# Kernel tuning notes

Measured on AMD Instinct MI355X. Metric: run time of the kernel, lower is better.

The kernel has to match this reference:

```python
import jax, jax.numpy as jnp
import numpy as np

N, E, B = 20000, 320000, 128
IN_DIM, HID, HEADS = 64, 64, 4
D = HID * HEADS          # 256 = conv output width (concat heads)
CAT = HID + 2 * D        # 576 = dueling head input
ENC_H, DUEL_H = 512, 128
NEG_SLOPE = 0.2


def setup_inputs() -> dict:
    key = jax.random.key(0)
    ks = jax.random.split(key, 30)
    g = lambda i, shape: jax.random.normal(ks[i], shape, dtype=jnp.float32) * 0.05
    return {
        "x": jax.random.normal(ks[0], (N, IN_DIM), dtype=jnp.float32),
        "edge_index": jax.random.randint(ks[1], (2, E), 0, N, dtype=jnp.int32),
        "indices": jax.random.randint(ks[2], (B,), 0, N, dtype=jnp.int32),
        # encoder MLP: input_dim -> 512 -> hidden_dim
        "enc_w1": g(3, (IN_DIM, ENC_H)), "enc_b1": g(4, (ENC_H,)),
        "enc_w2": g(5, (ENC_H, HID)),   "enc_b2": g(6, (HID,)),
        # GATv2 conv1: HID -> HID per head, HEADS heads
        "wl1": g(7, (HID, D)),  "bl1": g(8, (D,)),
        "wr1": g(9, (HID, D)),  "br1": g(10, (D,)),
        "att1": g(11, (HEADS, HID)), "bias1": g(12, (D,)),
        # GATv2 conv2: D -> HID per head, HEADS heads
        "wl2": g(13, (D, D)),   "bl2": g(14, (D,)),
        "wr2": g(15, (D, D)),   "br2": g(16, (D,)),
        "att2": g(17, (HEADS, HID)), "bias2": g(18, (D,)),
        # dueling heads: CAT -> 128 -> {2, 1}
        "q_w1": g(19, (CAT, DUEL_H)), "q_b1": g(20, (DUEL_H,)),
        "q_w2": g(21, (DUEL_H, 2)),   "q_b2": g(22, (2,)),
        "v_w1": g(23, (CAT, DUEL_H)), "v_b1": g(24, (DUEL_H,)),
        "v_w2": g(25, (DUEL_H, 1)),   "v_b2": g(26, (1,)),
    }


def _gatv2(h, src, dst, wl, bl, wr, br, att, bias):
    # PyG GATv2Conv: e_ij = att . leaky_relu(Wl h_j + Wr h_i); softmax over
    # incoming edges of each target i; out_i = sum_j alpha_ij * (Wl h_j).
    xl = (h @ wl + bl).reshape(-1, HEADS, HID)  # source transform
    xr = (h @ wr + br).reshape(-1, HEADS, HID)  # target transform
    e = jax.nn.leaky_relu(xl[src] + xr[dst], NEG_SLOPE)      # [E', H, D]
    score = jnp.einsum('ehd,hd->eh', e, att)                 # [E', H]
    m = jax.ops.segment_max(score, dst, num_segments=N)      # stable softmax
    ex = jnp.exp(score - m[dst])
    denom = jax.ops.segment_sum(ex, dst, num_segments=N)
    alpha = ex / (denom[dst] + 1e-16)                        # [E', H]
    out = jax.ops.segment_sum(alpha[:, :, None] * xl[src], dst, num_segments=N)
    return out.reshape(-1, D) + bias


def _forward(x, edge_index, indices,
             enc_w1, enc_b1, enc_w2, enc_b2,
             wl1, bl1, wr1, br1, att1, bias1,
             wl2, bl2, wr2, br2, att2, bias2,
             q_w1, q_b1, q_w2, q_b2, v_w1, v_b1, v_w2, v_b2):
    loops = jnp.arange(N, dtype=edge_index.dtype)  # add_self_loops=True
    src = jnp.concatenate([edge_index[0], loops])
    dst = jnp.concatenate([edge_index[1], loops])

    h = jax.nn.relu(x @ enc_w1 + enc_b1)
    h = jax.nn.relu(h @ enc_w2 + enc_b2)          # encoder + F.relu
    x1 = h[indices]
    h = jax.nn.relu(_gatv2(h, src, dst, wl1, bl1, wr1, br1, att1, bias1))
    x2 = h[indices]
    h = jax.nn.relu(_gatv2(h, src, dst, wl2, bl2, wr2, br2, att2, bias2))
    x3 = h[indices]

    feat = jnp.concatenate([x1, x2, x3], axis=1)  # [B, CAT]
    q = jax.nn.relu(feat @ q_w1 + q_b1) @ q_w2 + q_b2  # [B, 2]
    v = jax.nn.relu(feat @ v_w1 + v_b1) @ v_w2 + v_b2  # [B, 1]
    return q - q.mean(axis=1, keepdims=True) + v


def reference(x, edge_index, indices,
              enc_w1, enc_b1, enc_w2, enc_b2,
              wl1, bl1, wr1, br1, att1, bias1,
              wl2, bl2, wr2, br2, att2, bias2,
              q_w1, q_b1, q_w2, q_b2, v_w1, v_b1, v_w2, v_b2):
    return _forward(x, edge_index, indices,
                    enc_w1, enc_b1, enc_w2, enc_b2,
                    wl1, bl1, wr1, br1, att1, bias1,
                    wl2, bl2, wr2, br2, att2, bias2,
                    q_w1, q_b1, q_w2, q_b2, v_w1, v_b1, v_w2, v_b2)
```

## Files before the change

kernel.cpp:

```cpp
#include <hip/hip_runtime.h>

#define IN_DIM 64
#define HID 64
#define HEADS 4
#define DD 256
#define ENC_H 512
#define DUEL_H 128
#define NEG_SLOPE 0.2f
#define WCAP 8192
#define ECAP 64

typedef _Float16 f16;
typedef __attribute__((ext_vector_type(2))) _Float16 f16x2;
typedef __attribute__((ext_vector_type(4))) _Float16 f16x4;
typedef __attribute__((ext_vector_type(8))) _Float16 f16x8;
typedef __attribute__((ext_vector_type(4))) float f32x4;

__device__ __forceinline__ f16x2 u2h(unsigned u) {
    union { unsigned u; f16x2 h; } c; c.u = u; return c.h;
}
__device__ __forceinline__ unsigned h2u(f16x2 h) {
    union { unsigned u; f16x2 h; } c; c.h = h; return c.u;
}


__global__ void prep_all(
    const float4* __restrict__ x, f16x4* __restrict__ x16, int nx4,
    const float* __restrict__ w1, const float* __restrict__ w2,
    const float* __restrict__ wl1, const float* __restrict__ wr1,
    const float* __restrict__ wl2, const float* __restrict__ wr2,
    f16* __restrict__ w1t, f16* __restrict__ w2t,
    f16* __restrict__ wcat1, f16* __restrict__ wcat2,
    f16* __restrict__ wr2nt,
    int* __restrict__ zeros, int nz) {
    int i = blockIdx.x * blockDim.x + threadIdx.x;
    if (i < nx4) {
        float4 v = x[i];
        f16x4 o = {(f16)v.x, (f16)v.y, (f16)v.z, (f16)v.w};
        x16[i] = o;
        return;
    }
    i -= nx4;
    if (i < 229376) {
        if (i < 32768) {
            int k = i >> 9, n = i & 511;
            w1t[n * 64 + k] = (f16)w1[i];
        } else if (i < 65536) {
            int j = i - 32768; int k = j >> 6, n = j & 63;
            w2t[n * 512 + k] = (f16)w2[j];
        } else if (i < 81920) {
            int j = i - 65536; int k = j >> 8, n = j & 255;
            wcat1[n * 64 + k] = (f16)wl1[j];
        } else if (i < 98304) {
            int j = i - 81920; int k = j >> 8, n = j & 255;
            wcat1[(256 + n) * 64 + k] = (f16)wr1[j];
        } else if (i < 163840) {
            int j = i - 98304; int k = j >> 8, n = j & 255;
            wcat2[n * 256 + k] = (f16)wl2[j];
        } else {
            int j = i - 163840;
            wr2nt[j] = (f16)wr2[j];
        }
        return;
    }
    i -= 229376;
    if (i < nz) zeros[i] = 0;
}


template <int K, int BN>
struct GemmCfg {
    static constexpr int SB = K + 8;
    static constexpr int CE = BN / 2 + 8;
    static constexpr int SLABSZ = BN * SB;
    static constexpr int EPISZ = 4 * 32 * CE;
    static constexpr int SMEMSZ = SLABSZ > EPISZ ? SLABSZ : EPISZ;
};

template <int K, int BN>
__device__ __forceinline__ void gemm_body(
    int bx, int by, f16* __restrict__ smem,
    const f16* __restrict__ A, const f16* __restrict__ Bt,
    const float* __restrict__ biasA, const float* __restrict__ biasB, int NS,
    int M, int relu,
    f16* __restrict__ C1, f16* __restrict__ C2) {
    constexpr int KS = K / 32;
    constexpr int PF = (KS < 8) ? KS : 8;
    constexpr int COLW = BN / 2;
    constexpr int NT = COLW / 16;
    constexpr int SB = GemmCfg<K, BN>::SB;
    constexpr int CE = GemmCfg<K, BN>::CE;

    f16* Bs = smem;
    int tid = threadIdx.x;
    int wave = tid >> 6, lane = tid & 63;
    int quad = lane >> 4, l16 = lane & 15;
    int wr = wave >> 1, wc = wave & 1;
    int row0 = by * 64;
    int col0 = bx * BN;

    constexpr int NCH = BN * K / 8;
#pragma unroll
    for (int i = 0; i < NCH / 256; ++i) {
        int c = tid + i * 256;
        int r = c / (K / 8), ko = (c % (K / 8)) * 8;
        uint4 v = *(const uint4*)&Bt[(size_t)(col0 + r) * K + ko];
        *(uint4*)&Bs[r * SB + ko] = v;
    }
    __syncthreads();

    const f16* Aptr[2];
#pragma unroll
    for (int mt = 0; mt < 2; ++mt) {
        int arow = row0 + wr * 32 + mt * 16 + l16;
        if (arow >= M) arow = M - 1;
        Aptr[mt] = &A[(size_t)arow * K + quad * 8];
    }

    f32x4 acc[2][NT];
#pragma unroll
    for (int mt = 0; mt < 2; ++mt)
#pragma unroll
        for (int j = 0; j < NT; ++j) acc[mt][j] = (f32x4){0.f, 0.f, 0.f, 0.f};

    f16x8 afb[2][PF];
#pragma unroll
    for (int mt = 0; mt < 2; ++mt)
#pragma unroll
        for (int i = 0; i < PF; ++i)
            afb[mt][i] = *(const f16x8*)&Aptr[mt][i * 32];

#pragma unroll
    for (int s = 0; s < KS; ++s) {
        f16x8 af0 = afb[0][s % PF], af1 = afb[1][s % PF];
        if (s + PF < KS) {
            afb[0][s % PF] = *(const f16x8*)&Aptr[0][(s + PF) * 32];
            afb[1][s % PF] = *(const f16x8*)&Aptr[1][(s + PF) * 32];
        }
        const f16* bbase = &Bs[(size_t)(wc * COLW) * SB + s * 32 + quad * 8];
#pragma unroll
        for (int nt = 0; nt < NT; ++nt) {
            f16x8 bf = *(const f16x8*)&bbase[(nt * 16 + l16) * SB];
            acc[0][nt] = __builtin_amdgcn_mfma_f32_16x16x32_f16(af0, bf, acc[0][nt], 0, 0, 0);
            acc[1][nt] = __builtin_amdgcn_mfma_f32_16x16x32_f16(af1, bf, acc[1][nt], 0, 0, 0);
        }
    }

    __syncthreads();
    f16* ep = &smem[wave * 32 * CE];
#pragma unroll
    for (int mt = 0; mt < 2; ++mt)
#pragma unroll
        for (int nt = 0; nt < NT; ++nt) {
            int gcol = col0 + wc * COLW + nt * 16 + l16;
            float bb = (gcol < NS) ? biasA[gcol] : biasB[gcol - NS];
#pragma unroll
            for (int r = 0; r < 4; ++r) {
                float v = acc[mt][nt][r] + bb;
                if (relu) v = fmaxf(v, 0.f);
                ep[(mt * 16 + quad * 4 + r) * CE + nt * 16 + l16] = (f16)v;
            }
        }
    constexpr int CPR = COLW / 8;
    constexpr int NPASS = (32 * CPR) / 64;
#pragma unroll
    for (int i = 0; i < NPASS; ++i) {
        int u = lane + i * 64;
        int row = u / CPR, seg = u % CPR;
        uint4 v = *(const uint4*)&ep[row * CE + seg * 8];
        int grow = row0 + wr * 32 + row;
        int gcol = col0 + wc * COLW + seg * 8;
        if (grow < M) {
            if (gcol < NS) *(uint4*)&C1[(size_t)grow * NS + gcol] = v;
            else           *(uint4*)&C2[(size_t)grow * NS + (gcol - NS)] = v;
        }
    }
}


__global__ __launch_bounds__(256) void conv2t_gather_kernel(
    const f16* __restrict__ A, const f16* __restrict__ Bt,
    const float* __restrict__ bias,
    const int* __restrict__ wlist, const int* __restrict__ wcnt,
    f16* __restrict__ C) {
    constexpr int K = 256, BN = 128;
    constexpr int KS = K / 32, PF = 8;
    constexpr int COLW = BN / 2, NT = COLW / 16;
    constexpr int SB = GemmCfg<K, BN>::SB;
    constexpr int CE = GemmCfg<K, BN>::CE;
    __shared__ __align__(16) f16 smem[GemmCfg<K, BN>::SMEMSZ];

    int M_c = wcnt[0];
    int row0 = blockIdx.y * 64;
    if (row0 >= M_c) return;

    f16* Bs = smem;
    int tid = threadIdx.x;
    int wave = tid >> 6, lane = tid & 63;
    int quad = lane >> 4, l16 = lane & 15;
    int wr = wave >> 1, wc = wave & 1;
    int col0 = blockIdx.x * BN;

    constexpr int NCH = BN * K / 8;
#pragma unroll
    for (int i = 0; i < NCH / 256; ++i) {
        int c = tid + i * 256;
        int r = c / (K / 8), ko = (c % (K / 8)) * 8;
        uint4 v = *(const uint4*)&Bt[(size_t)(col0 + r) * K + ko];
        *(uint4*)&Bs[r * SB + ko] = v;
    }
    __syncthreads();

    const f16* Aptr[2];
#pragma unroll
    for (int mt = 0; mt < 2; ++mt) {
        int crow = row0 + wr * 32 + mt * 16 + l16;
        if (crow >= M_c) crow = M_c - 1;
        int arow = wlist[crow];
        Aptr[mt] = &A[(size_t)arow * K + quad * 8];
    }

    f32x4 acc[2][NT];
#pragma unroll
    for (int mt = 0; mt < 2; ++mt)
#pragma unroll
        for (int j = 0; j < NT; ++j) acc[mt][j] = (f32x4){0.f, 0.f, 0.f, 0.f};

    f16x8 afb[2][PF];
#pragma unroll
    for (int mt = 0; mt < 2; ++mt)
#pragma unroll
        for (int i = 0; i < PF; ++i)
            afb[mt][i] = *(const f16x8*)&Aptr[mt][i * 32];

#pragma unroll
    for (int s = 0; s < KS; ++s) {
        f16x8 af0 = afb[0][s % PF], af1 = afb[1][s % PF];
        const f16* bbase = &Bs[(size_t)(wc * COLW) * SB + s * 32 + quad * 8];
#pragma unroll
        for (int nt = 0; nt < NT; ++nt) {
            f16x8 bf = *(const f16x8*)&bbase[(nt * 16 + l16) * SB];
            acc[0][nt] = __builtin_amdgcn_mfma_f32_16x16x32_f16(af0, bf, acc[0][nt], 0, 0, 0);
            acc[1][nt] = __builtin_amdgcn_mfma_f32_16x16x32_f16(af1, bf, acc[1][nt], 0, 0, 0);
        }
    }

    __syncthreads();
    f16* ep = &smem[wave * 32 * CE];
#pragma unroll
    for (int mt = 0; mt < 2; ++mt)
#pragma unroll
        for (int nt = 0; nt < NT; ++nt) {
            int gcol = col0 + wc * COLW + nt * 16 + l16;
            float bb = bias[gcol];
#pragma unroll
            for (int r = 0; r < 4; ++r)
                ep[(mt * 16 + quad * 4 + r) * CE + nt * 16 + l16] =
                    (f16)(acc[mt][nt][r] + bb);
        }
    constexpr int CPR = COLW / 8;
    constexpr int NPASS = (32 * CPR) / 64;
#pragma unroll
    for (int i = 0; i < NPASS; ++i) {
        int u = lane + i * 64;
        int row = u / CPR, seg = u % CPR;
        uint4 v = *(const uint4*)&ep[row * CE + seg * 8];
        int grow = row0 + wr * 32 + row;
        int gcol = col0 + wc * COLW + seg * 8;
        if (grow < M_c) *(uint4*)&C[(size_t)grow * DD + gcol] = v;
    }
}


__device__ __forceinline__ void wappend(int src, int* __restrict__ inW,
                                        int* __restrict__ wcnt,
                                        int* __restrict__ wlist,
                                        int* __restrict__ mapv,
                                        int* __restrict__ w_edges,
                                        int* __restrict__ ecnt) {
    if (atomicExch(&inW[src], 1) == 0) {
        int c = atomicAdd(wcnt, 1);
        if (c < WCAP) {
            wlist[c] = src;
            mapv[src] = c;
            w_edges[c * ECAP] = src;
            ecnt[c] = 1;
        }
    }
}

__global__ __launch_bounds__(256) void enc1_s0_kernel(
    const f16* __restrict__ A, const f16* __restrict__ Bt,
    const float* __restrict__ bias, int M, f16* __restrict__ C, int gemmBlocks,
    const int* __restrict__ indices, int B,
    int* __restrict__ s0f, int* __restrict__ inW, int* __restrict__ wcnt,
    int* __restrict__ wlist, int* __restrict__ mapv,
    int* __restrict__ w_edges, int* __restrict__ ecnt) {
    __shared__ __align__(16) f16 smem[GemmCfg<64, 128>::SMEMSZ];
    int bid = blockIdx.x;
    if (bid >= gemmBlocks) {
        int t = threadIdx.x;
        if (t < B) {
            int src = indices[t];
            s0f[src] = 1;
            wappend(src, inW, wcnt, wlist, mapv, w_edges, ecnt);
        }
        return;
    }
    gemm_body<64, 128>(bid & 3, bid >> 2, smem, A, Bt, bias, bias, 512, M, 1, C, C);
}

__global__ __launch_bounds__(256) void enc2_wscan_kernel(
    const f16* __restrict__ A, const f16* __restrict__ Bt,
    const float* __restrict__ bias, int M, f16* __restrict__ C, int gemmBlocks,
    const int* __restrict__ ei, int E,
    const int* __restrict__ s0f, int* __restrict__ inW, int* __restrict__ wcnt,
    int* __restrict__ wlist, int* __restrict__ mapv,
    int* __restrict__ w_edges, int* __restrict__ ecnt) {
    __shared__ __align__(16) f16 smem[GemmCfg<512, 64>::SMEMSZ];
    int bid = blockIdx.x;
    if (bid < gemmBlocks) {
        gemm_body<512, 64>(0, bid, smem, A, Bt, bias, bias, 64, M, 1, C, C);
    } else {
        int e = (bid - gemmBlocks) * 256 + threadIdx.x;
        if (e < E) {
            int dst = ei[E + e];
            if (s0f[dst])
                wappend(ei[e], inW, wcnt, wlist, mapv, w_edges, ecnt);
        }
    }
}

__global__ __launch_bounds__(256) void conv1t_ebuild_kernel(
    const f16* __restrict__ A, const f16* __restrict__ Bt,
    const float* __restrict__ biasA, const float* __restrict__ biasB, int M,
    f16* __restrict__ C1, f16* __restrict__ C2, int gemmBlocks,
    const int* __restrict__ ei, int E,
    const int* __restrict__ inW, const int* __restrict__ mapv,
    int* __restrict__ w_edges, int* __restrict__ ecnt) {
    __shared__ __align__(16) f16 smem[GemmCfg<64, 128>::SMEMSZ];
    int bid = blockIdx.x;
    if (bid < gemmBlocks) {
        gemm_body<64, 128>(bid & 3, bid >> 2, smem, A, Bt, biasA, biasB, DD, M, 0, C1, C2);
    } else {
        int e = (bid - gemmBlocks) * 256 + threadIdx.x;
        if (e < E) {
            int dst = ei[E + e];
            if (inW[dst]) {
                int c = mapv[dst];
                int pos = atomicAdd(&ecnt[c], 1);
                if (pos < ECAP) w_edges[c * ECAP + pos] = ei[e];
            }
        }
    }
}


__global__ __launch_bounds__(256) void gat_fused_kernel(
    const uint4* __restrict__ xl, const uint4* __restrict__ xr,
    const float4* __restrict__ att,
    const int* __restrict__ wlist, const int* __restrict__ wcnt,
    const int* __restrict__ w_edges, const int* __restrict__ ecnt,
    const float4* __restrict__ bias, uint4* __restrict__ h16) {
    int w = (blockIdx.x * blockDim.x + threadIdx.x) >> 6;
    int lane = threadIdx.x & 63;
    int half = lane >> 5, l32 = lane & 31;
    if (w >= wcnt[0]) return;
    int node = wlist[w];
    int L = ecnt[w];
    if (L > ECAP) L = ECAP;
    const int* elist = &w_edges[w * ECAP];
    uint4 xrw = xr[(size_t)node * 32 + l32];
    f16x2 xr0 = u2h(xrw.x), xr1 = u2h(xrw.y), xr2 = u2h(xrw.z), xr3 = u2h(xrw.w);
    float4 awA = att[l32 * 2], awB = att[l32 * 2 + 1];
    f16x2 a6[4] = {{(f16)(0.6f * awA.x), (f16)(0.6f * awA.y)},
                   {(f16)(0.6f * awA.z), (f16)(0.6f * awA.w)},
                   {(f16)(0.6f * awB.x), (f16)(0.6f * awB.y)},
                   {(f16)(0.6f * awB.z), (f16)(0.6f * awB.w)}};
    f16x2 a4[4] = {{(f16)(0.4f * awA.x), (f16)(0.4f * awA.y)},
                   {(f16)(0.4f * awA.z), (f16)(0.4f * awA.w)},
                   {(f16)(0.4f * awB.x), (f16)(0.4f * awB.y)},
                   {(f16)(0.4f * awB.z), (f16)(0.4f * awB.w)}};
    float denom = 0.f;
    float acc0 = 0.f, acc1 = 0.f, acc2 = 0.f, acc3 = 0.f;
    float acc4 = 0.f, acc5 = 0.f, acc6 = 0.f, acc7 = 0.f;

    auto edge_dot = [&](uint4 raw) -> float {
        f16x2 t0 = u2h(raw.x) + xr0, t1 = u2h(raw.y) + xr1;
        f16x2 t2 = u2h(raw.z) + xr2, t3 = u2h(raw.w) + xr3;
        float d = __builtin_amdgcn_fdot2(t0, a6[0], 0.f, false);
        d = __builtin_amdgcn_fdot2(u2h(h2u(t0) & 0x7FFF7FFFu), a4[0], d, false);
        d = __builtin_amdgcn_fdot2(t1, a6[1], d, false);
        d = __builtin_amdgcn_fdot2(u2h(h2u(t1) & 0x7FFF7FFFu), a4[1], d, false);
        d = __builtin_amdgcn_fdot2(t2, a6[2], d, false);
        d = __builtin_amdgcn_fdot2(u2h(h2u(t2) & 0x7FFF7FFFu), a4[2], d, false);
        d = __builtin_amdgcn_fdot2(t3, a6[3], d, false);
        d = __builtin_amdgcn_fdot2(u2h(h2u(t3) & 0x7FFF7FFFu), a4[3], d, false);
        return d;
    };
    auto accum = [&](uint4 raw, float ee) {
        f16x2 v0 = u2h(raw.x), v1 = u2h(raw.y), v2 = u2h(raw.z), v3 = u2h(raw.w);
        acc0 = fmaf(ee, (float)v0.x, acc0); acc1 = fmaf(ee, (float)v0.y, acc1);
        acc2 = fmaf(ee, (float)v1.x, acc2); acc3 = fmaf(ee, (float)v1.y, acc3);
        acc4 = fmaf(ee, (float)v2.x, acc4); acc5 = fmaf(ee, (float)v2.y, acc5);
        acc6 = fmaf(ee, (float)v3.x, acc6); acc7 = fmaf(ee, (float)v3.y, acc7);
    };

    int p = half;
    for (; p + 6 < L; p += 8) {
        uint4 raw[4];
#pragma unroll
        for (int j = 0; j < 4; ++j)
            raw[j] = xl[(size_t)elist[p + j * 2] * 32 + l32];
        float sc[4];
#pragma unroll
        for (int j = 0; j < 4; ++j) sc[j] = edge_dot(raw[j]);
#pragma unroll
        for (int j = 0; j < 4; ++j) sc[j] += __shfl_xor(sc[j], 1);
#pragma unroll
        for (int j = 0; j < 4; ++j) sc[j] += __shfl_xor(sc[j], 2);
#pragma unroll
        for (int j = 0; j < 4; ++j) sc[j] += __shfl_xor(sc[j], 4);
#pragma unroll
        for (int j = 0; j < 4; ++j) {
            float ee = __expf(sc[j]);
            denom += ee;
            accum(raw[j], ee);
        }
    }
    for (; p < L; p += 2) {
        uint4 raw = xl[(size_t)elist[p] * 32 + l32];
        float d = edge_dot(raw);
        d += __shfl_xor(d, 1);
        d += __shfl_xor(d, 2);
        d += __shfl_xor(d, 4);
        float ee = __expf(d);
        denom += ee;
        accum(raw, ee);
    }
    denom += __shfl_xor(denom, 32);
    acc0 += __shfl_xor(acc0, 32); acc1 += __shfl_xor(acc1, 32);
    acc2 += __shfl_xor(acc2, 32); acc3 += __shfl_xor(acc3, 32);
    acc4 += __shfl_xor(acc4, 32); acc5 += __shfl_xor(acc5, 32);
    acc6 += __shfl_xor(acc6, 32); acc7 += __shfl_xor(acc7, 32);

    if (half == 0) {
        float inv = 1.f / (denom + 1e-16f);
        float4 bbA = bias[l32 * 2], bbB = bias[l32 * 2 + 1];
        float o0 = fmaxf(fmaf(acc0, inv, bbA.x), 0.f);
        float o1 = fmaxf(fmaf(acc1, inv, bbA.y), 0.f);
        float o2 = fmaxf(fmaf(acc2, inv, bbA.z), 0.f);
        float o3 = fmaxf(fmaf(acc3, inv, bbA.w), 0.f);
        float o4 = fmaxf(fmaf(acc4, inv, bbB.x), 0.f);
        float o5 = fmaxf(fmaf(acc5, inv, bbB.y), 0.f);
        float o6 = fmaxf(fmaf(acc6, inv, bbB.z), 0.f);
        float o7 = fmaxf(fmaf(acc7, inv, bbB.w), 0.f);
        f16x2 h0 = {(f16)o0, (f16)o1}, h1 = {(f16)o2, (f16)o3};
        f16x2 h2 = {(f16)o4, (f16)o5}, h3 = {(f16)o6, (f16)o7};
        uint4 outw = make_uint4(h2u(h0), h2u(h1), h2u(h2), h2u(h3));
        h16[(size_t)node * 32 + l32] = outw;
    }
}


__global__ __launch_bounds__(1024) void gat2_head_kernel(
    const uint4* __restrict__ xl, const f16* __restrict__ hC1,
    const f16* __restrict__ wr2nt, const float* __restrict__ br2,
    const float4* __restrict__ att,
    const int* __restrict__ indices, const int* __restrict__ mapv,
    const int* __restrict__ w_edges, const int* __restrict__ ecnt,
    const float* __restrict__ bias2, const f16* __restrict__ hE16,
    const float* __restrict__ qw1, const float* __restrict__ qb1,
    const float* __restrict__ qw2, const float* __restrict__ qb2,
    const float* __restrict__ vw1, const float* __restrict__ vb1,
    const float* __restrict__ vw2, const float* __restrict__ vb2,
    float* __restrict__ out) {
    __shared__ float feat[576];
    __shared__ float xrs[256];
    __shared__ float partial[4][256];
    __shared__ float pden[16][32];
    __shared__ float pacc[16][32][8];
    __shared__ float red[384];
    int b = blockIdx.x;
    int t = threadIdx.x;
    int wave = t >> 6, lane = t & 63;
    int half = lane >> 5, l32 = lane & 31;
    int node = indices[b];

    if (t < 320) {
        feat[t] = (t < 64) ? (float)hE16[(size_t)node * 64 + t]
                           : (float)hC1[(size_t)node * 256 + t - 64];
    }
    __syncthreads();

    {
        int o = t & 255, kq = t >> 8;
        const f16* w = &wr2nt[(size_t)(kq * 64) * 256 + o];
        const float* f = &feat[64 + kq * 64];
        float a0 = 0.f, a1 = 0.f;
#pragma unroll
        for (int k = 0; k < 64; k += 2) {
            a0 = fmaf(f[k],     (float)w[(size_t)k * 256],       a0);
            a1 = fmaf(f[k + 1], (float)w[(size_t)(k + 1) * 256], a1);
        }
        partial[kq][o] = a0 + a1;
    }
    __syncthreads();
    if (t < 256)
        xrs[t] = partial[0][t] + partial[1][t] + partial[2][t] + partial[3][t] + br2[t];
    __syncthreads();

    f16x2 xr0 = {(f16)xrs[l32 * 8 + 0], (f16)xrs[l32 * 8 + 1]};
    f16x2 xr1 = {(f16)xrs[l32 * 8 + 2], (f16)xrs[l32 * 8 + 3]};
    f16x2 xr2 = {(f16)xrs[l32 * 8 + 4], (f16)xrs[l32 * 8 + 5]};
    f16x2 xr3 = {(f16)xrs[l32 * 8 + 6], (f16)xrs[l32 * 8 + 7]};

    int cidx0 = mapv[node];
    int L = ecnt[cidx0];
    if (L > ECAP) L = ECAP;
    const int* elist = &w_edges[cidx0 * ECAP];
    float4 awA = att[l32 * 2], awB = att[l32 * 2 + 1];
    f16x2 a6[4] = {{(f16)(0.6f * awA.x), (f16)(0.6f * awA.y)},
                   {(f16)(0.6f * awA.z), (f16)(0.6f * awA.w)},
                   {(f16)(0.6f * awB.x), (f16)(0.6f * awB.y)},
                   {(f16)(0.6f * awB.z), (f16)(0.6f * awB.w)}};
    f16x2 a4[4] = {{(f16)(0.4f * awA.x), (f16)(0.4f * awA.y)},
                   {(f16)(0.4f * awA.z), (f16)(0.4f * awA.w)},
                   {(f16)(0.4f * awB.x), (f16)(0.4f * awB.y)},
                   {(f16)(0.4f * awB.z), (f16)(0.4f * awB.w)}};
    float denom = 0.f;
    float acc0 = 0.f, acc1 = 0.f, acc2 = 0.f, acc3 = 0.f;
    float acc4 = 0.f, acc5 = 0.f, acc6 = 0.f, acc7 = 0.f;

    auto edge_dot = [&](uint4 raw) -> float {
        f16x2 t0 = u2h(raw.x) + xr0, t1 = u2h(raw.y) + xr1;
        f16x2 t2 = u2h(raw.z) + xr2, t3 = u2h(raw.w) + xr3;
        float d = __builtin_amdgcn_fdot2(t0, a6[0], 0.f, false);
        d = __builtin_amdgcn_fdot2(u2h(h2u(t0) & 0x7FFF7FFFu), a4[0], d, false);
        d = __builtin_amdgcn_fdot2(t1, a6[1], d, false);
        d = __builtin_amdgcn_fdot2(u2h(h2u(t1) & 0x7FFF7FFFu), a4[1], d, false);
        d = __builtin_amdgcn_fdot2(t2, a6[2], d, false);
        d = __builtin_amdgcn_fdot2(u2h(h2u(t2) & 0x7FFF7FFFu), a4[2], d, false);
        d = __builtin_amdgcn_fdot2(t3, a6[3], d, false);
        d = __builtin_amdgcn_fdot2(u2h(h2u(t3) & 0x7FFF7FFFu), a4[3], d, false);
        return d;
    };
    auto accum = [&](uint4 raw, float ee) {
        f16x2 v0 = u2h(raw.x), v1 = u2h(raw.y), v2 = u2h(raw.z), v3 = u2h(raw.w);
        acc0 = fmaf(ee, (float)v0.x, acc0); acc1 = fmaf(ee, (float)v0.y, acc1);
        acc2 = fmaf(ee, (float)v1.x, acc2); acc3 = fmaf(ee, (float)v1.y, acc3);
        acc4 = fmaf(ee, (float)v2.x, acc4); acc5 = fmaf(ee, (float)v2.y, acc5);
        acc6 = fmaf(ee, (float)v3.x, acc6); acc7 = fmaf(ee, (float)v3.y, acc7);
    };

    for (int p = (wave << 1) + half; p < L; p += 32) {
        int cidx = mapv[elist[p]];
        uint4 raw = xl[(size_t)cidx * 32 + l32];
        float d = edge_dot(raw);
        d += __shfl_xor(d, 1);
        d += __shfl_xor(d, 2);
        d += __shfl_xor(d, 4);
        float ee = __expf(d);
        denom += ee;
        accum(raw, ee);
    }
    denom += __shfl_xor(denom, 32);
    acc0 += __shfl_xor(acc0, 32); acc1 += __shfl_xor(acc1, 32);
    acc2 += __shfl_xor(acc2, 32); acc3 += __shfl_xor(acc3, 32);
    acc4 += __shfl_xor(acc4, 32); acc5 += __shfl_xor(acc5, 32);
    acc6 += __shfl_xor(acc6, 32); acc7 += __shfl_xor(acc7, 32);
    if (half == 0) {
        pden[wave][l32] = denom;
        pacc[wave][l32][0] = acc0; pacc[wave][l32][1] = acc1;
        pacc[wave][l32][2] = acc2; pacc[wave][l32][3] = acc3;
        pacc[wave][l32][4] = acc4; pacc[wave][l32][5] = acc5;
        pacc[wave][l32][6] = acc6; pacc[wave][l32][7] = acc7;
    }
    __syncthreads();

    if (t < 256) {
        int lw = t >> 3, d = t & 7;
        float den = 0.f, a = 0.f;
#pragma unroll
        for (int w = 0; w < 16; ++w) { den += pden[w][lw]; a += pacc[w][lw][d]; }
        float inv = 1.f / (den + 1e-16f);
        feat[320 + t] = fmaxf(fmaf(a, inv, bias2[t]), 0.f);
    }
    __syncthreads();

    {
        int o = t & 255, kq = t >> 8;
        int k0 = kq * 144;
        float a0 = 0.f, a1 = 0.f;
        if (o < 128) {
            const float* w = &qw1[(size_t)k0 * 128 + o];
            const float* f = &feat[k0];
#pragma unroll
            for (int k = 0; k < 144; k += 2) {
                a0 = fmaf(f[k],     w[(size_t)k * 128],       a0);
                a1 = fmaf(f[k + 1], w[(size_t)(k + 1) * 128], a1);
            }
        } else {
            const float* w = &vw1[(size_t)k0 * 128 + (o - 128)];
            const float* f = &feat[k0];
#pragma unroll
            for (int k = 0; k < 144; k += 2) {
                a0 = fmaf(f[k],     w[(size_t)k * 128],       a0);
                a1 = fmaf(f[k + 1], w[(size_t)(k + 1) * 128], a1);
            }
        }
        partial[kq][o] = a0 + a1;
    }
    __syncthreads();
    if (t < 256) {
        float s4 = partial[0][t] + partial[1][t] + partial[2][t] + partial[3][t];
        if (t < 128) {
            float aq = fmaxf(s4 + qb1[t], 0.f);
            red[t]       = aq * qw2[t * 2 + 0];
            red[128 + t] = aq * qw2[t * 2 + 1];
        } else {
            int tv = t - 128;
            float av = fmaxf(s4 + vb1[tv], 0.f);
            red[256 + tv] = av * vw2[tv];
        }
    }
    __syncthreads();
    for (int s2 = 64; s2 > 0; s2 >>= 1) {
        if (t < s2) {
            red[t] += red[t + s2];
            red[128 + t] += red[128 + t + s2];
            red[256 + t] += red[256 + t + s2];
        }
        __syncthreads();
    }
    if (t == 0) {
        float q0 = red[0] + qb2[0];
        float q1 = red[128] + qb2[1];
        float v  = red[256] + vb2[0];
        float mean = 0.5f * (q0 + q1);
        out[b * 2 + 0] = q0 - mean + v;
        out[b * 2 + 1] = q1 - mean + v;
    }
}


extern "C" void kernel_launch(void* const* d_in, const int* in_sizes, int n_in,
                              void* d_out, int out_size, void* d_ws, size_t ws_size,
                              hipStream_t stream) {
    const float* x      = (const float*)d_in[0];
    const int*   ei     = (const int*)d_in[1];
    const int*   indices= (const int*)d_in[2];
    const float* enc_w1 = (const float*)d_in[3];
    const float* enc_b1 = (const float*)d_in[4];
    const float* enc_w2 = (const float*)d_in[5];
    const float* enc_b2 = (const float*)d_in[6];
    const float* wl1    = (const float*)d_in[7];
    const float* bl1    = (const float*)d_in[8];
    const float* wr1    = (const float*)d_in[9];
    const float* br1    = (const float*)d_in[10];
    const float* att1   = (const float*)d_in[11];
    const float* bias1  = (const float*)d_in[12];
    const float* wl2    = (const float*)d_in[13];
    const float* bl2    = (const float*)d_in[14];
    const float* wr2    = (const float*)d_in[15];
    const float* br2    = (const float*)d_in[16];
    const float* att2   = (const float*)d_in[17];
    const float* bias2  = (const float*)d_in[18];
    const float* qw1    = (const float*)d_in[19];
    const float* qb1    = (const float*)d_in[20];
    const float* qw2    = (const float*)d_in[21];
    const float* qb2    = (const float*)d_in[22];
    const float* vw1    = (const float*)d_in[23];
    const float* vb1    = (const float*)d_in[24];
    const float* vw2    = (const float*)d_in[25];
    const float* vb2    = (const float*)d_in[26];

    const int N = in_sizes[0] / IN_DIM;
    const int E = in_sizes[1] / 2;
    const int B = in_sizes[2];

    char* wsb = (char*)d_ws;
    size_t off = 0;
    auto alloc = [&](size_t bytes) -> void* {
        void* p = wsb + off;
        off = (off + bytes + 255) & ~(size_t)255;
        return p;
    };
    f16* x16     = (f16*)alloc((size_t)N * 64 * 2);
    f16* h1_16   = (f16*)alloc((size_t)N * 512 * 2);
    f16* hE16    = (f16*)alloc((size_t)N * 64 * 2);
    f16* xl16    = (f16*)alloc((size_t)N * 256 * 2);
    f16* xr16    = (f16*)alloc((size_t)N * 256 * 2);
    f16* hC1_16  = (f16*)alloc((size_t)N * 256 * 2);
    f16* w1t     = (f16*)alloc((size_t)ENC_H * IN_DIM * 2);
    f16* w2t     = (f16*)alloc((size_t)HID * ENC_H * 2);
    f16* wcat1   = (f16*)alloc((size_t)512 * HID * 2);
    f16* wcat2   = (f16*)alloc((size_t)256 * DD * 2);
    f16* wr2nt   = (f16*)alloc((size_t)DD * DD * 2);
    int* zeros   = (int*)alloc((size_t)(2 * N + 16) * 4);
    int* s0f     = zeros;
    int* inW     = s0f + N;
    int* wcnt    = inW + N;
    int* wlist   = (int*)alloc((size_t)WCAP * 4);
    int* mapv    = (int*)alloc((size_t)N * 4);
    int* ecnt    = (int*)alloc((size_t)WCAP * 4);
    int* w_edges = (int*)alloc((size_t)WCAP * ECAP * 4);

    int nx4 = N * 16;
    int nz = 2 * N + 16;
    int ntot = nx4 + 229376 + nz;
    prep_all<<<(ntot + 255) / 256, 256, 0, stream>>>(
        (const float4*)x, (f16x4*)x16, nx4,
        enc_w1, enc_w2, wl1, wr1, wl2, wr2,
        w1t, w2t, wcat1, wcat2, wr2nt, zeros, nz);

    int grows = (N + 63) / 64;
    int gemmB1 = 4 * grows;
    int escanB = (E + 255) / 256;

    enc1_s0_kernel<<<gemmB1 + 1, 256, 0, stream>>>(
        x16, w1t, enc_b1, N, h1_16, gemmB1,
        indices, B, s0f, inW, wcnt, wlist, mapv, w_edges, ecnt);

    enc2_wscan_kernel<<<grows + escanB, 256, 0, stream>>>(
        h1_16, w2t, enc_b2, N, hE16, grows,
        ei, E, s0f, inW, wcnt, wlist, mapv, w_edges, ecnt);

    conv1t_ebuild_kernel<<<gemmB1 + escanB, 256, 0, stream>>>(
        hE16, wcat1, bl1, br1, N, xl16, xr16, gemmB1,
        ei, E, inW, mapv, w_edges, ecnt);

    gat_fused_kernel<<<(WCAP * 64) / 256, 256, 0, stream>>>(
        (const uint4*)xl16, (const uint4*)xr16, (const float4*)att1,
        wlist, wcnt, w_edges, ecnt, (const float4*)bias1, (uint4*)hC1_16);

    conv2t_gather_kernel<<<dim3(2, WCAP / 64), dim3(256), 0, stream>>>(
        hC1_16, wcat2, bl2, wlist, wcnt, xl16);

    gat2_head_kernel<<<B, 1024, 0, stream>>>(
        (const uint4*)xl16, hC1_16, wr2nt, br2, (const float4*)att2,
        indices, mapv, w_edges, ecnt, bias2, hE16,
        qw1, qb1, qw2, qb2, vw1, vb1, vw2, vb2, (float*)d_out);
}
```

Measured before the change: 183.4 us.

## Fuse conv2 source transform into GAT1 aggregation kernel via shared-memory rows

```diff
diff --git a/kernel.cpp b/kernel.cpp
--- a/kernel.cpp
+++ b/kernel.cpp
@@ -178,100 +178,6 @@
 }
 
 
-__global__ __launch_bounds__(256) void conv2t_gather_kernel(
-    const f16* __restrict__ A, const f16* __restrict__ Bt,
-    const float* __restrict__ bias,
-    const int* __restrict__ wlist, const int* __restrict__ wcnt,
-    f16* __restrict__ C) {
-    constexpr int K = 256, BN = 128;
-    constexpr int KS = K / 32, PF = 8;
-    constexpr int COLW = BN / 2, NT = COLW / 16;
-    constexpr int SB = GemmCfg<K, BN>::SB;
-    constexpr int CE = GemmCfg<K, BN>::CE;
-    __shared__ __align__(16) f16 smem[GemmCfg<K, BN>::SMEMSZ];
-
-    int M_c = wcnt[0];
-    int row0 = blockIdx.y * 64;
-    if (row0 >= M_c) return;
-
-    f16* Bs = smem;
-    int tid = threadIdx.x;
-    int wave = tid >> 6, lane = tid & 63;
-    int quad = lane >> 4, l16 = lane & 15;
-    int wr = wave >> 1, wc = wave & 1;
-    int col0 = blockIdx.x * BN;
-
-    constexpr int NCH = BN * K / 8;
-#pragma unroll
-    for (int i = 0; i < NCH / 256; ++i) {
-        int c = tid + i * 256;
-        int r = c / (K / 8), ko = (c % (K / 8)) * 8;
-        uint4 v = *(const uint4*)&Bt[(size_t)(col0 + r) * K + ko];
-        *(uint4*)&Bs[r * SB + ko] = v;
-    }
-    __syncthreads();
-
-    const f16* Aptr[2];
-#pragma unroll
-    for (int mt = 0; mt < 2; ++mt) {
-        int crow = row0 + wr * 32 + mt * 16 + l16;
-        if (crow >= M_c) crow = M_c - 1;
-        int arow = wlist[crow];
-        Aptr[mt] = &A[(size_t)arow * K + quad * 8];
-    }
-
-    f32x4 acc[2][NT];
-#pragma unroll
-    for (int mt = 0; mt < 2; ++mt)
-#pragma unroll
-        for (int j = 0; j < NT; ++j) acc[mt][j] = (f32x4){0.f, 0.f, 0.f, 0.f};
-
-    f16x8 afb[2][PF];
-#pragma unroll
-    for (int mt = 0; mt < 2; ++mt)
-#pragma unroll
-        for (int i = 0; i < PF; ++i)
-            afb[mt][i] = *(const f16x8*)&Aptr[mt][i * 32];
-
-#pragma unroll
-    for (int s = 0; s < KS; ++s) {
-        f16x8 af0 = afb[0][s % PF], af1 = afb[1][s % PF];
-        const f16* bbase = &Bs[(size_t)(wc * COLW) * SB + s * 32 + quad * 8];
-#pragma unroll
-        for (int nt = 0; nt < NT; ++nt) {
-            f16x8 bf = *(const f16x8*)&bbase[(nt * 16 + l16) * SB];
-            acc[0][nt] = __builtin_amdgcn_mfma_f32_16x16x32_f16(af0, bf, acc[0][nt], 0, 0, 0);
-            acc[1][nt] = __builtin_amdgcn_mfma_f32_16x16x32_f16(af1, bf, acc[1][nt], 0, 0, 0);
-        }
-    }
-
-    __syncthreads();
-    f16* ep = &smem[wave * 32 * CE];
-#pragma unroll
-    for (int mt = 0; mt < 2; ++mt)
-#pragma unroll
-        for (int nt = 0; nt < NT; ++nt) {
-            int gcol = col0 + wc * COLW + nt * 16 + l16;
-            float bb = bias[gcol];
-#pragma unroll
-            for (int r = 0; r < 4; ++r)
-                ep[(mt * 16 + quad * 4 + r) * CE + nt * 16 + l16] =
-                    (f16)(acc[mt][nt][r] + bb);
-        }
-    constexpr int CPR = COLW / 8;
-    constexpr int NPASS = (32 * CPR) / 64;
-#pragma unroll
-    for (int i = 0; i < NPASS; ++i) {
-        int u = lane + i * 64;
-        int row = u / CPR, seg = u % CPR;
-        uint4 v = *(const uint4*)&ep[row * CE + seg * 8];
-        int grow = row0 + wr * 32 + row;
-        int gcol = col0 + wc * COLW + seg * 8;
-        if (grow < M_c) *(uint4*)&C[(size_t)grow * DD + gcol] = v;
-    }
-}
-
-
 __device__ __forceinline__ void wappend(int src, int* __restrict__ inW,
                                         int* __restrict__ wcnt,
                                         int* __restrict__ wlist,
@@ -356,20 +262,28 @@
 }
 
 
-__global__ __launch_bounds__(256) void gat_fused_kernel(
+__global__ __launch_bounds__(256) void gat1_conv2t_kernel(
     const uint4* __restrict__ xl, const uint4* __restrict__ xr,
     const float4* __restrict__ att,
     const int* __restrict__ wlist, const int* __restrict__ wcnt,
     const int* __restrict__ w_edges, const int* __restrict__ ecnt,
-    const float4* __restrict__ bias, uint4* __restrict__ h16) {
-    int w = (blockIdx.x * blockDim.x + threadIdx.x) >> 6;
-    int lane = threadIdx.x & 63;
+    const float4* __restrict__ bias, uint4* __restrict__ h16,
+    const f16* __restrict__ wcat2, const float* __restrict__ bl2,
+    f16* __restrict__ xl2) {
+    __shared__ f16 rowbuf[4][264];
+    int wc0 = wcnt[0];
+    if (wc0 > WCAP) wc0 = WCAP;
+    int tid = threadIdx.x;
+    int w = (blockIdx.x * blockDim.x + tid) >> 6;
+    int lane = tid & 63;
+    int wave = tid >> 6;
     int half = lane >> 5, l32 = lane & 31;
-    if (w >= wcnt[0]) return;
-    int node = wlist[w];
-    int L = ecnt[w];
+    bool active = (w < wc0);
+    int wi = active ? w : 0;
+    int node = wlist[wi];
+    int L = active ? ecnt[wi] : 0;
     if (L > ECAP) L = ECAP;
-    const int* elist = &w_edges[w * ECAP];
+    const int* elist = &w_edges[wi * ECAP];
     uint4 xrw = xr[(size_t)node * 32 + l32];
     f16x2 xr0 = u2h(xrw.x), xr1 = u2h(xrw.y), xr2 = u2h(xrw.z), xr3 = u2h(xrw.w);
     float4 awA = att[l32 * 2], awB = att[l32 * 2 + 1];
@@ -444,21 +358,54 @@
     acc4 += __shfl_xor(acc4, 32); acc5 += __shfl_xor(acc5, 32);
     acc6 += __shfl_xor(acc6, 32); acc7 += __shfl_xor(acc7, 32);
 
+    float inv = 1.f / (denom + 1e-16f);
+    float4 bbA = bias[l32 * 2], bbB = bias[l32 * 2 + 1];
+    float o0 = fmaxf(fmaf(acc0, inv, bbA.x), 0.f);
+    float o1 = fmaxf(fmaf(acc1, inv, bbA.y), 0.f);
+    float o2 = fmaxf(fmaf(acc2, inv, bbA.z), 0.f);
+    float o3 = fmaxf(fmaf(acc3, inv, bbA.w), 0.f);
+    float o4 = fmaxf(fmaf(acc4, inv, bbB.x), 0.f);
+    float o5 = fmaxf(fmaf(acc5, inv, bbB.y), 0.f);
+    float o6 = fmaxf(fmaf(acc6, inv, bbB.z), 0.f);
+    float o7 = fmaxf(fmaf(acc7, inv, bbB.w), 0.f);
+    f16x2 h0 = {(f16)o0, (f16)o1}, h1 = {(f16)o2, (f16)o3};
+    f16x2 h2 = {(f16)o4, (f16)o5}, h3 = {(f16)o6, (f16)o7};
     if (half == 0) {
-        float inv = 1.f / (denom + 1e-16f);
-        float4 bbA = bias[l32 * 2], bbB = bias[l32 * 2 + 1];
-        float o0 = fmaxf(fmaf(acc0, inv, bbA.x), 0.f);
-        float o1 = fmaxf(fmaf(acc1, inv, bbA.y), 0.f);
-        float o2 = fmaxf(fmaf(acc2, inv, bbA.z), 0.f);
-        float o3 = fmaxf(fmaf(acc3, inv, bbA.w), 0.f);
-        float o4 = fmaxf(fmaf(acc4, inv, bbB.x), 0.f);
-        float o5 = fmaxf(fmaf(acc5, inv, bbB.y), 0.f);
-        float o6 = fmaxf(fmaf(acc6, inv, bbB.z), 0.f);
-        float o7 = fmaxf(fmaf(acc7, inv, bbB.w), 0.f);
-        f16x2 h0 = {(f16)o0, (f16)o1}, h1 = {(f16)o2, (f16)o3};
-        f16x2 h2 = {(f16)o4, (f16)o5}, h3 = {(f16)o6, (f16)o7};
-        uint4 outw = make_uint4(h2u(h0), h2u(h1), h2u(h2), h2u(h3));
-        h16[(size_t)node * 32 + l32] = outw;
+        f16* rb = &rowbuf[wave][l32 * 8];
+        rb[0] = h0.x; rb[1] = h0.y; rb[2] = h1.x; rb[3] = h1.y;
+        rb[4] = h2.x; rb[5] = h2.y; rb[6] = h3.x; rb[7] = h3.y;
+        if (active) {
+            uint4 outw = make_uint4(h2u(h0), h2u(h1), h2u(h2), h2u(h3));
+            h16[(size_t)node * 32 + l32] = outw;
+        }
+    }
+    __syncthreads();
+
+    int wbase = blockIdx.x * 4;
+    bool wact[4];
+#pragma unroll
+    for (int v = 0; v < 4; ++v) wact[v] = (wbase + v) < wc0;
+    {
+        int c = tid;
+        float a0c = 0.f, a1c = 0.f, a2c = 0.f, a3c = 0.f;
+        const f16* wcol = &wcat2[(size_t)c * 256];
+#pragma unroll 4
+        for (int k = 0; k < 256; k += 8) {
+            f16x8 wv = *(const f16x8*)&wcol[k];
+#pragma unroll
+            for (int j = 0; j < 8; ++j) {
+                float wj = (float)wv[j];
+                a0c = fmaf((float)rowbuf[0][k + j], wj, a0c);
+                a1c = fmaf((float)rowbuf[1][k + j], wj, a1c);
+                a2c = fmaf((float)rowbuf[2][k + j], wj, a2c);
+                a3c = fmaf((float)rowbuf[3][k + j], wj, a3c);
+            }
+        }
+        float bb = bl2[c];
+        if (wact[0]) xl2[(size_t)(wbase + 0) * DD + c] = (f16)(a0c + bb);
+        if (wact[1]) xl2[(size_t)(wbase + 1) * DD + c] = (f16)(a1c + bb);
+        if (wact[2]) xl2[(size_t)(wbase + 2) * DD + c] = (f16)(a2c + bb);
+        if (wact[3]) xl2[(size_t)(wbase + 3) * DD + c] = (f16)(a3c + bb);
     }
 }
 
@@ -692,6 +639,7 @@
     f16* xl16    = (f16*)alloc((size_t)N * 256 * 2);
     f16* xr16    = (f16*)alloc((size_t)N * 256 * 2);
     f16* hC1_16  = (f16*)alloc((size_t)N * 256 * 2);
+    f16* xl2c    = (f16*)alloc((size_t)WCAP * 256 * 2);
     f16* w1t     = (f16*)alloc((size_t)ENC_H * IN_DIM * 2);
     f16* w2t     = (f16*)alloc((size_t)HID * ENC_H * 2);
     f16* wcat1   = (f16*)alloc((size_t)512 * HID * 2);
@@ -730,15 +678,13 @@
         hE16, wcat1, bl1, br1, N, xl16, xr16, gemmB1,
         ei, E, inW, mapv, w_edges, ecnt);
 
-    gat_fused_kernel<<<(WCAP * 64) / 256, 256, 0, stream>>>(
+    gat1_conv2t_kernel<<<(WCAP * 64) / 256, 256, 0, stream>>>(
         (const uint4*)xl16, (const uint4*)xr16, (const float4*)att1,
-        wlist, wcnt, w_edges, ecnt, (const float4*)bias1, (uint4*)hC1_16);
-
-    conv2t_gather_kernel<<<dim3(2, WCAP / 64), dim3(256), 0, stream>>>(
-        hC1_16, wcat2, bl2, wlist, wcnt, xl16);
+        wlist, wcnt, w_edges, ecnt, (const float4*)bias1, (uint4*)hC1_16,
+        wcat2, bl2, xl2c);
 
     gat2_head_kernel<<<B, 1024, 0, stream>>>(
-        (const uint4*)xl16, hC1_16, wr2nt, br2, (const float4*)att2,
+        (const uint4*)xl2c, hC1_16, wr2nt, br2, (const float4*)att2,
         indices, mapv, w_edges, ecnt, bias2, hE16,
         qw1, qb1, qw2, qb2, vw1, vb1, vw2, vb2, (float*)d_out);
 }
```

After: 222.8 us. +21.5%, slower.
